# Performance work log

Measured on AMD Instinct MI355X. Metric: run time of the kernel, lower is better.

The kernel has to match this reference:

```python
import jax, jax.numpy as jnp
import numpy as np
from jax import lax

KERNEL = 3
K = 3


def setup_inputs() -> dict:
    key = jax.random.key(0)
    xcorr = jax.random.normal(key, (16, 1, 256, 8192), dtype=jnp.float32)
    return {"xcorr": xcorr}


def reference(xcorr):
    # xcorr: [B, C, H, W] (W = lag axis)
    W = xcorr.shape[-1]
    nlag = W // 2
    # max_pool2d with kernel (1,KERNEL), stride 1, padding (0, KERNEL//2).
    # torch pads with -inf for max pooling.
    neg_inf = jnp.asarray(-jnp.inf, dtype=xcorr.dtype)
    pad = KERNEL // 2
    smax = lax.reduce_window(
        xcorr,
        neg_inf,
        lax.max,
        window_dimensions=(1, 1, 1, KERNEL),
        window_strides=(1, 1, 1, 1),
        padding=[(0, 0), (0, 0), (0, 0), (pad, pad)],
    )
    keep = (smax == xcorr).astype(xcorr.dtype)  # local-max NMS mask
    scores = xcorr * keep
    topk_scores, topk_inds = lax.top_k(scores, K)  # sorted descending, [B,C,H,K]
    top = topk_inds[..., 0]  # best peak index [B,C,H]
    nearby = jnp.clip(
        jnp.stack([top - 1, top, top + 1], axis=-1), 0, W - 1
    )  # [B,C,H,3]
    neighbor_score = jnp.take_along_axis(xcorr, nearby, axis=-1)
    topk_index = topk_inds - nlag
    return neighbor_score, topk_scores, topk_index
```

## Files before the change

### kernel.cpp

```cpp
#include <hip/hip_runtime.h>
#include <climits>
#include <cmath>


#define PW    8192
#define PNLAG (PW / 2)
#define BLOCK 256
#define NW    4
#define J     8

__device__ __forceinline__ bool better(float av, int ai, float bv, int bi) {
  return (av > bv) || ((av == bv) && (ai < bi));
}

__device__ __forceinline__ void insert3_full(float v, int i,
                                             float &v0, int &i0,
                                             float &v1, int &i1,
                                             float &v2, int &i2) {
  if (better(v, i, v2, i2)) {
    if (better(v, i, v1, i1)) {
      if (better(v, i, v0, i0)) {
        v2 = v1; i2 = i1; v1 = v0; i1 = i0; v0 = v; i0 = i;
      } else {
        v2 = v1; i2 = i1; v1 = v; i1 = i;
      }
    } else {
      v2 = v; i2 = i;
    }
  }
}

__device__ __forceinline__ void insert3_fast(float c, int ci,
                                             float &v0, int &i0,
                                             float &v1, int &i1,
                                             float &v2, int &i2) {
  const bool b2 = c > v2;
  const bool b1 = c > v1;
  const bool b0 = c > v0;
  v2 = b1 ? v1 : (b2 ? c : v2);  i2 = b1 ? i1 : (b2 ? ci : i2);
  v1 = b0 ? v0 : (b1 ? c : v1);  i1 = b0 ? i0 : (b1 ? ci : i1);
  v0 = b0 ? c  : v0;             i0 = b0 ? ci : i0;
}

__global__ __launch_bounds__(BLOCK, 4)
void detect_peaks_kernel(const float* __restrict__ x,
                         float* __restrict__ out,
                         int rows) {
  __shared__ float rv[NW * 3];
  __shared__ int   ri[NW * 3];

  const int row  = blockIdx.x;
  const int t    = threadIdx.x;
  const int lane = t & 63;
  const int wave = t >> 6;
  const float* __restrict__ xr = x + (size_t)row * PW;

  const int span = J * 64 * 4;
  const int base = wave * span;

  float4 q[J];
#pragma unroll
  for (int j = 0; j < J; ++j)
    q[j] = *(const float4*)(xr + base + (j * 64 + lane) * 4);

  const float edgeL = (base > 0)         ? xr[base - 1]    : -INFINITY;
  const float edgeR = (base + span < PW) ? xr[base + span] : -INFINITY;

  float v0 = -INFINITY, v1 = -INFINITY, v2 = -INFINITY;
  int   i0 = INT_MAX,   i1 = INT_MAX,   i2 = INT_MAX;

#pragma unroll
  for (int j = 0; j < J; ++j) {
    const float4 v = q[j];

    float left = __shfl_up(v.w, 1);
    const float lf = (j == 0) ? edgeL : __shfl(q[j - 1].w, 63);
    if (lane == 0) left = lf;
    float right = __shfl_down(v.x, 1);
    const float rf = (j == J - 1) ? edgeR : __shfl(q[j + 1].x, 0);
    if (lane == 63) right = rf;

    const int p = base + (j * 64 + lane) * 4;

    const float p01 = fmaxf(v.x, v.y);
    const float p12 = fmaxf(v.y, v.z);
    const float p23 = fmaxf(v.z, v.w);
    const float m0 = fmaxf(left, p01);
    const float m1 = fmaxf(p01, v.z);
    const float m2 = fmaxf(p12, v.w);
    const float m3 = fmaxf(p23, right);

    const float s0 = (v.x == m0) ? v.x : 0.0f;
    const float s1 = (v.y == m1) ? v.y : 0.0f;
    const float s2 = (v.z == m2) ? v.z : 0.0f;
    const float s3 = (v.w == m3) ? v.w : 0.0f;

    const bool  a01 = s0 >= s1;
    const float hiA = a01 ? s0 : s1;   const int hiAi = a01 ? p     : p + 1;
    const float loA = a01 ? s1 : s0;   const int loAi = a01 ? p + 1 : p;
    const bool  a23 = s2 >= s3;
    const float hiB = a23 ? s2 : s3;   const int hiBi = a23 ? p + 2 : p + 3;
    const float loB = a23 ? s3 : s2;   const int loBi = a23 ? p + 3 : p + 2;

    const bool  ab  = hiA >= hiB;
    const float c1  = ab ? hiA : hiB;  const int c1i = ab ? hiAi : hiBi;
    const bool  sb  = ab ? (loA >= hiB) : (hiA >= loB);
    const float c2  = ab ? (sb ? loA : hiB) : (sb ? hiA : loB);
    const int   c2i = ab ? (sb ? loAi : hiBi) : (sb ? hiAi : loBi);

    insert3_fast(c1, c1i, v0, i0, v1, i1, v2, i2);
    insert3_fast(c2, c2i, v0, i0, v1, i1, v2, i2);
  }

#pragma unroll
  for (int off = 32; off > 0; off >>= 1) {
    float ov0 = __shfl_down(v0, off);
    int   oi0 = __shfl_down(i0, off);
    float ov1 = __shfl_down(v1, off);
    int   oi1 = __shfl_down(i1, off);
    float ov2 = __shfl_down(v2, off);
    int   oi2 = __shfl_down(i2, off);
    if (lane + off < 64) {
      insert3_full(ov0, oi0, v0, i0, v1, i1, v2, i2);
      insert3_full(ov1, oi1, v0, i0, v1, i1, v2, i2);
      insert3_full(ov2, oi2, v0, i0, v1, i1, v2, i2);
    }
  }

  if (lane == 0) {
    rv[wave * 3 + 0] = v0; ri[wave * 3 + 0] = i0;
    rv[wave * 3 + 1] = v1; ri[wave * 3 + 1] = i1;
    rv[wave * 3 + 2] = v2; ri[wave * 3 + 2] = i2;
  }
  __syncthreads();

  if (t == 0) {
#pragma unroll
    for (int w = 1; w < NW; ++w) {
      insert3_full(rv[w * 3 + 0], ri[w * 3 + 0], v0, i0, v1, i1, v2, i2);
      insert3_full(rv[w * 3 + 1], ri[w * 3 + 1], v0, i0, v1, i1, v2, i2);
      insert3_full(rv[w * 3 + 2], ri[w * 3 + 2], v0, i0, v1, i1, v2, i2);
    }

    float* __restrict__ nb = out;
    float* __restrict__ ts = out + (size_t)rows * 3;
    float* __restrict__ ti = out + (size_t)rows * 6;

    const int top = i0;
#pragma unroll
    for (int k = 0; k < 3; ++k) {
      int idx = top - 1 + k;
      idx = idx < 0 ? 0 : (idx > PW - 1 ? PW - 1 : idx);
      nb[row * 3 + k] = xr[idx];
    }
    ts[row * 3 + 0] = v0;
    ts[row * 3 + 1] = v1;
    ts[row * 3 + 2] = v2;
    ti[row * 3 + 0] = (float)(i0 - PNLAG);
    ti[row * 3 + 1] = (float)(i1 - PNLAG);
    ti[row * 3 + 2] = (float)(i2 - PNLAG);
  }
}

extern "C" void kernel_launch(void* const* d_in, const int* in_sizes, int n_in,
                              void* d_out, int out_size, void* d_ws, size_t ws_size,
                              hipStream_t stream) {
  const float* x = (const float*)d_in[0];
  float* out = (float*)d_out;
  const int rows = in_sizes[0] / PW;
  detect_peaks_kernel<<<rows, BLOCK, 0, stream>>>(x, out, rows);
}
```

Before: 240.5 us.

## Split peak detection into per-chunk pass and separate merge kernel

Measured after the change: 243.5 us. About the same (+1.3%).

```diff
diff --git a/kernel.cpp b/kernel.cpp
--- a/kernel.cpp
+++ b/kernel.cpp
@@ -8,6 +8,8 @@
 #define BLOCK 256
 #define NW    4
 #define J     8
+#define CHUNK 2048
+#define CPR   4
 
 __device__ __forceinline__ bool better(float av, int ai, float bv, int bi) {
   return (av > bv) || ((av == bv) && (ai < bi));
@@ -43,28 +45,23 @@
 }
 
 __global__ __launch_bounds__(BLOCK, 4)
-void detect_peaks_kernel(const float* __restrict__ x,
-                         float* __restrict__ out,
-                         int rows) {
-  __shared__ float rv[NW * 3];
-  __shared__ int   ri[NW * 3];
+void peaks_pass1(const float* __restrict__ x, float* __restrict__ ws) {
+  const int t     = threadIdx.x;
+  const int lane  = t & 63;
+  const int wave  = t >> 6;
+  const int chunk = blockIdx.x * NW + wave;
+  const int row   = chunk >> 2;
+  const int c     = chunk & 3;
+  const float* __restrict__ xr = x + (size_t)row * PW;
+  const int base  = c * CHUNK;
 
-  const int row  = blockIdx.x;
-  const int t    = threadIdx.x;
-  const int lane = t & 63;
-  const int wave = t >> 6;
-  const float* __restrict__ xr = x + (size_t)row * PW;
-
-  const int span = J * 64 * 4;
-  const int base = wave * span;
+  const float edgeL = (base > 0)          ? xr[base - 1]     : -INFINITY;
+  const float edgeR = (base + CHUNK < PW) ? xr[base + CHUNK] : -INFINITY;
 
   float4 q[J];
 #pragma unroll
   for (int j = 0; j < J; ++j)
     q[j] = *(const float4*)(xr + base + (j * 64 + lane) * 4);
-
-  const float edgeL = (base > 0)         ? xr[base - 1]    : -INFINITY;
-  const float edgeR = (base + span < PW) ? xr[base + span] : -INFINITY;
 
   float v0 = -INFINITY, v1 = -INFINITY, v2 = -INFINITY;
   int   i0 = INT_MAX,   i1 = INT_MAX,   i2 = INT_MAX;
@@ -128,38 +125,51 @@
   }
 
   if (lane == 0) {
-    rv[wave * 3 + 0] = v0; ri[wave * 3 + 0] = i0;
-    rv[wave * 3 + 1] = v1; ri[wave * 3 + 1] = i1;
-    rv[wave * 3 + 2] = v2; ri[wave * 3 + 2] = i2;
+    float* o = ws + (size_t)chunk * 8;
+    float4 vv; vv.x = v0; vv.y = v1; vv.z = v2; vv.w = 0.0f;
+    *(float4*)o = vv;
+    int4 ii; ii.x = i0; ii.y = i1; ii.z = i2; ii.w = 0;
+    *(int4*)(o + 4) = ii;
   }
-  __syncthreads();
+}
 
-  if (t == 0) {
+__global__ __launch_bounds__(BLOCK)
+void peaks_pass2(const float* __restrict__ x, const float* __restrict__ ws,
+                 float* __restrict__ out, int rows) {
+  const int row = blockIdx.x * BLOCK + threadIdx.x;
+  if (row >= rows) return;
+
+  float v0 = -INFINITY, v1 = -INFINITY, v2 = -INFINITY;
+  int   i0 = INT_MAX,   i1 = INT_MAX,   i2 = INT_MAX;
+
 #pragma unroll
-    for (int w = 1; w < NW; ++w) {
-      insert3_full(rv[w * 3 + 0], ri[w * 3 + 0], v0, i0, v1, i1, v2, i2);
-      insert3_full(rv[w * 3 + 1], ri[w * 3 + 1], v0, i0, v1, i1, v2, i2);
-      insert3_full(rv[w * 3 + 2], ri[w * 3 + 2], v0, i0, v1, i1, v2, i2);
-    }
+  for (int c = 0; c < CPR; ++c) {
+    const float* o = ws + ((size_t)row * CPR + c) * 8;
+    const float4 vv = *(const float4*)o;
+    const int4   ii = *(const int4*)(o + 4);
+    insert3_full(vv.x, ii.x, v0, i0, v1, i1, v2, i2);
+    insert3_full(vv.y, ii.y, v0, i0, v1, i1, v2, i2);
+    insert3_full(vv.z, ii.z, v0, i0, v1, i1, v2, i2);
+  }
 
-    float* __restrict__ nb = out;
-    float* __restrict__ ts = out + (size_t)rows * 3;
-    float* __restrict__ ti = out + (size_t)rows * 6;
+  const float* __restrict__ xr = x + (size_t)row * PW;
+  float* __restrict__ nb = out;
+  float* __restrict__ ts = out + (size_t)rows * 3;
+  float* __restrict__ ti = out + (size_t)rows * 6;
 
-    const int top = i0;
+  const int top = i0;
 #pragma unroll
-    for (int k = 0; k < 3; ++k) {
-      int idx = top - 1 + k;
-      idx = idx < 0 ? 0 : (idx > PW - 1 ? PW - 1 : idx);
-      nb[row * 3 + k] = xr[idx];
-    }
-    ts[row * 3 + 0] = v0;
-    ts[row * 3 + 1] = v1;
-    ts[row * 3 + 2] = v2;
-    ti[row * 3 + 0] = (float)(i0 - PNLAG);
-    ti[row * 3 + 1] = (float)(i1 - PNLAG);
-    ti[row * 3 + 2] = (float)(i2 - PNLAG);
+  for (int k = 0; k < 3; ++k) {
+    int idx = top - 1 + k;
+    idx = idx < 0 ? 0 : (idx > PW - 1 ? PW - 1 : idx);
+    nb[row * 3 + k] = xr[idx];
   }
+  ts[row * 3 + 0] = v0;
+  ts[row * 3 + 1] = v1;
+  ts[row * 3 + 2] = v2;
+  ti[row * 3 + 0] = (float)(i0 - PNLAG);
+  ti[row * 3 + 1] = (float)(i1 - PNLAG);
+  ti[row * 3 + 2] = (float)(i2 - PNLAG);
 }
 
 extern "C" void kernel_launch(void* const* d_in, const int* in_sizes, int n_in,
@@ -167,6 +177,9 @@
                               hipStream_t stream) {
   const float* x = (const float*)d_in[0];
   float* out = (float*)d_out;
+  float* ws  = (float*)d_ws;
   const int rows = in_sizes[0] / PW;
-  detect_peaks_kernel<<<rows, BLOCK, 0, stream>>>(x, out, rows);
+
+  peaks_pass1<<<rows * CPR / NW, BLOCK, 0, stream>>>(x, ws);
+  peaks_pass2<<<(rows + BLOCK - 1) / BLOCK, BLOCK, 0, stream>>>(x, ws, out, rows);
 }
```
